# Performance work log

Hardware: AMD Instinct MI355X
Metric: run time of the kernel (lower is better)

Reference implementation:

```python
import jax, jax.numpy as jnp
import numpy as np

N = 50000   # nodes
E = 600000  # edges
H = 128     # hidden_dim


def _linear_params(key, fan_in, fan_out):
    kw, kb = jax.random.split(key)
    s = 1.0 / np.sqrt(fan_in)
    w = jax.random.uniform(kw, (fan_in, fan_out), minval=-s, maxval=s, dtype=jnp.float32)
    b = jax.random.uniform(kb, (fan_out,), minval=-s, maxval=s, dtype=jnp.float32)
    return w, b


def setup_inputs():
    key = jax.random.key(0)
    ks = jax.random.split(key, 9)
    x = jax.random.uniform(ks[0], (N, 1), dtype=jnp.float32)
    pre_h = jax.random.normal(ks[1], (N, H), dtype=jnp.float32)
    edge_index = jax.random.randint(ks[2], (2, E), 0, N, dtype=jnp.int32)
    edge_attr = jax.random.uniform(ks[3], (E, 1), dtype=jnp.float32)
    enc_w, enc_b = _linear_params(ks[4], 1 + H, H)      # BFS_Encoder.linear
    M_w, M_b = _linear_params(ks[5], H + H + 1, H)      # MPNN_Processor.M
    U_w, U_b = _linear_params(ks[6], H + H, H)          # MPNN_Processor.U
    dec_w, dec_b = _linear_params(ks[7], H + H, 1)      # BFS_Decoder.linear
    ter_w, ter_b = _linear_params(ks[8], H + H, 1)      # BFS_Terminator.linear
    return {"x": x, "pre_h": pre_h, "edge_attr": edge_attr,
            "enc_w": enc_w, "enc_b": enc_b, "M_w": M_w, "M_b": M_b,
            "U_w": U_w, "U_b": U_b, "dec_w": dec_w, "dec_b": dec_b,
            "ter_w": ter_w, "ter_b": ter_b, "edge_index": edge_index}


def reference(x, pre_h, edge_attr, enc_w, enc_b, M_w, M_b, U_w, U_b,
              dec_w, dec_b, ter_w, ter_b, edge_index):
    # Encoder: z = relu(Linear([x, pre_h]))
    z = jax.nn.relu(jnp.concatenate([x, pre_h], axis=-1) @ enc_w + enc_b)  # [N,H]

    # Processor (PyG MessagePassing, flow source_to_target):
    # z_i = z[edge_index[1]] (target), z_j = z[edge_index[0]] (source)
    src, tgt = edge_index[0], edge_index[1]
    m = jax.nn.relu(
        jnp.concatenate([z[tgt], z[src], edge_attr], axis=-1) @ M_w + M_b)  # [E,H]
    # scatter-max aggregate into target nodes; empty segments -> 0
    agg = jax.ops.segment_max(m, tgt, num_segments=N)
    agg = jnp.where(jnp.isfinite(agg), agg, 0.0)
    h = jax.nn.relu(jnp.concatenate([z, agg], axis=-1) @ U_w + U_b)  # [N,H]

    # Decoder
    y = jax.nn.sigmoid(jnp.concatenate([z, h], axis=-1) @ dec_w + dec_b)  # [N,1]

    # Terminator: mean over nodes, broadcast-concat, scalar mean
    h_mean = jnp.broadcast_to(jnp.mean(h, axis=0), h.shape)
    ter = jnp.mean(jnp.concatenate([h, h_mean], axis=-1) @ ter_w + ter_b)
    return h, y, ter
```

## Files before the change

### kernel.cpp

```cpp
#include <hip/hip_runtime.h>
#include <hip/hip_bf16.h>
#include <math.h>

#define HD 128
#define APAD 136
#define CAP 768

typedef short bf16x8 __attribute__((ext_vector_type(8)));
typedef float f32x4 __attribute__((ext_vector_type(4)));

static __device__ __forceinline__ unsigned short f2bf(float f) {
  __hip_bfloat16 b = __float2bfloat16(f);
  return *(unsigned short*)&b;
}
static __device__ __forceinline__ float bflo(unsigned int u) {
  return __uint_as_float(u << 16);
}
static __device__ __forceinline__ float bfhi(unsigned int u) {
  return __uint_as_float(u & 0xffff0000u);
}

__global__ __launch_bounds__(256) void k_frag(
    const float* __restrict__ enc_w, const float* __restrict__ M_w,
    const float* __restrict__ U_w,
    unsigned short* __restrict__ encf, unsigned short* __restrict__ Pf,
    unsigned short* __restrict__ Qf, unsigned short* __restrict__ Uf) {
  const int b = blockIdx.x;
  const float* W; unsigned short* F; int KS; int lb;
  if (b < 8)       { W = enc_w + HD;     F = encf; KS = 4; lb = b; }
  else if (b < 16) { W = M_w;            F = Pf;   KS = 4; lb = b - 8; }
  else if (b < 24) { W = M_w + HD * HD;  F = Qf;   KS = 4; lb = b - 16; }
  else             { W = U_w;            F = Uf;   KS = 8; lb = b - 24; }
  const int gid = lb * 256 + threadIdx.x;
  const int lane = gid & 63;
  const int ks = (gid >> 6) % KS;
  const int tile = gid / (64 * KS);
  const int col = tile * 16 + (lane & 15);
  const int k0 = ks * 32 + (lane >> 4) * 8;
  unsigned short v[8];
#pragma unroll
  for (int j = 0; j < 8; ++j) v[j] = f2bf(W[(size_t)(k0 + j) * HD + col]);
  unsigned short* dst = F + ((size_t)(tile * KS + ks) * 64 + lane) * 8;
#pragma unroll
  for (int j = 0; j < 8; ++j) dst[j] = v[j];
}

__global__ __launch_bounds__(256) void k_hist(
    const int* __restrict__ ei, int* __restrict__ cnt, int E) {
  const int e = blockIdx.x * 256 + threadIdx.x;
  if (e < E) atomicAdd(&cnt[ei[E + e]], 1);
}

__global__ __launch_bounds__(256) void k_scan_block(
    const int* __restrict__ cnt, int* __restrict__ row_ptr,
    int* __restrict__ partials, int N) {
  __shared__ int s[256];
  const int t = threadIdx.x;
  const int base = blockIdx.x * 1024 + t * 4;
  int v[4], sum = 0;
#pragma unroll
  for (int i = 0; i < 4; ++i) {
    v[i] = (base + i < N) ? cnt[base + i] : 0;
    sum += v[i];
  }
  s[t] = sum;
  __syncthreads();
  for (int off = 1; off < 256; off <<= 1) {
    int xv = (t >= off) ? s[t - off] : 0;
    __syncthreads();
    if (t >= off) s[t] += xv;
    __syncthreads();
  }
  int run = s[t] - sum;
  if (t == 255) partials[blockIdx.x] = s[255];
#pragma unroll
  for (int i = 0; i < 4; ++i) {
    if (base + i < N) row_ptr[base + i] = run;
    run += v[i];
  }
}

__global__ void k_scan_partials(int* __restrict__ partials, int nb) {
  if (threadIdx.x == 0) {
    int run = 0;
    for (int i = 0; i < nb; ++i) { int v = partials[i]; partials[i] = run; run += v; }
  }
}

__global__ __launch_bounds__(256) void k_scan_add(
    int* __restrict__ row_ptr, const int* __restrict__ partials,
    int* __restrict__ cursor, int N) {
  const int base = blockIdx.x * 1024 + threadIdx.x * 4;
  const int p = partials[blockIdx.x];
#pragma unroll
  for (int i = 0; i < 4; ++i) {
    if (base + i < N) {
      int v = row_ptr[base + i] + p;
      row_ptr[base + i] = v;
      cursor[base + i] = v;
    }
  }
}

__global__ __launch_bounds__(256) void k_scatter(
    const int* __restrict__ ei, const float* __restrict__ edge_attr,
    int* __restrict__ cursor, int2* __restrict__ epack, int E) {
  const int e = blockIdx.x * 256 + threadIdx.x;
  if (e >= E) return;
  const int tgt = ei[E + e];
  const int pos = atomicAdd(&cursor[tgt], 1);
  epack[pos] = make_int2(ei[e], __float_as_int(edge_attr[e]));
}

__global__ __launch_bounds__(256, 4) void k_enc_pq(
    const float* __restrict__ x, const float* __restrict__ pre_h,
    const float* __restrict__ enc_w, const float* __restrict__ enc_b,
    const float* __restrict__ M_b,
    const unsigned short* __restrict__ encf, const unsigned short* __restrict__ Pf,
    const unsigned short* __restrict__ Qf,
    unsigned short* __restrict__ zg, unsigned short* __restrict__ Pg,
    unsigned short* __restrict__ Qg) {
  __shared__ unsigned short phs[16 * APAD];
  __shared__ unsigned short zsh[16 * APAD];
  __shared__ float xs[16];
  const int t = threadIdx.x;
  const int n0 = blockIdx.x * 16;

  {
    const int r = t >> 4, c0 = (t & 15) * 8;
    const float4 a = *(const float4*)&pre_h[(size_t)(n0 + r) * HD + c0];
    const float4 b = *(const float4*)&pre_h[(size_t)(n0 + r) * HD + c0 + 4];
    unsigned short* d = &phs[r * APAD + c0];
    d[0] = f2bf(a.x); d[1] = f2bf(a.y); d[2] = f2bf(a.z); d[3] = f2bf(a.w);
    d[4] = f2bf(b.x); d[5] = f2bf(b.y); d[6] = f2bf(b.z); d[7] = f2bf(b.w);
  }
  if (t < 16) xs[t] = x[n0 + t];
  __syncthreads();

  const int w = t >> 6, l = t & 63;
  const int m = l & 15, q = l >> 4;

  bf16x8 af[4];
#pragma unroll
  for (int ks = 0; ks < 4; ++ks)
    af[ks] = *(const bf16x8*)&phs[m * APAD + ks * 32 + q * 8];
  f32x4 acc[2] = {{0, 0, 0, 0}, {0, 0, 0, 0}};
#pragma unroll
  for (int tt = 0; tt < 2; ++tt) {
    const int tn = 2 * w + tt;
#pragma unroll
    for (int ks = 0; ks < 4; ++ks) {
      const bf16x8 bf = *(const bf16x8*)&encf[((size_t)(tn * 4 + ks) * 64 + l) * 8];
      acc[tt] = __builtin_amdgcn_mfma_f32_16x16x32_bf16(af[ks], bf, acc[tt], 0, 0, 0);
    }
  }
#pragma unroll
  for (int tt = 0; tt < 2; ++tt) {
    const int col = (2 * w + tt) * 16 + m;
    const float bb = enc_b[col];
    const float w0 = enc_w[col];
#pragma unroll
    for (int r = 0; r < 4; ++r) {
      const int row = q * 4 + r;
      const float zv = fmaxf(acc[tt][r] + bb + xs[row] * w0, 0.0f);
      zsh[row * APAD + col] = f2bf(zv);
    }
  }
  __syncthreads();

  bf16x8 az[4];
#pragma unroll
  for (int ks = 0; ks < 4; ++ks)
    az[ks] = *(const bf16x8*)&zsh[m * APAD + ks * 32 + q * 8];
  {
    const int r = t >> 4, c0 = (t & 15) * 8;
    *(uint4*)&zg[(size_t)(n0 + r) * HD + c0] = *(const uint4*)&zsh[r * APAD + c0];
  }
  __syncthreads();

  f32x4 pacc[2] = {{0, 0, 0, 0}, {0, 0, 0, 0}};
  f32x4 qacc[2] = {{0, 0, 0, 0}, {0, 0, 0, 0}};
#pragma unroll
  for (int tt = 0; tt < 2; ++tt) {
    const int tn = 2 * w + tt;
#pragma unroll
    for (int ks = 0; ks < 4; ++ks) {
      const bf16x8 bp = *(const bf16x8*)&Pf[((size_t)(tn * 4 + ks) * 64 + l) * 8];
      const bf16x8 bq = *(const bf16x8*)&Qf[((size_t)(tn * 4 + ks) * 64 + l) * 8];
      pacc[tt] = __builtin_amdgcn_mfma_f32_16x16x32_bf16(az[ks], bp, pacc[tt], 0, 0, 0);
      qacc[tt] = __builtin_amdgcn_mfma_f32_16x16x32_bf16(az[ks], bq, qacc[tt], 0, 0, 0);
    }
  }
#pragma unroll
  for (int tt = 0; tt < 2; ++tt) {
    const int col = (2 * w + tt) * 16 + m;
    const float mb = M_b[col];
#pragma unroll
    for (int r = 0; r < 4; ++r) {
      const int row = q * 4 + r;
      phs[row * APAD + col] = f2bf(pacc[tt][r] + mb);
      zsh[row * APAD + col] = f2bf(qacc[tt][r]);
    }
  }
  __syncthreads();
  {
    const int r = t >> 4, c0 = (t & 15) * 8;
    *(uint4*)&Pg[(size_t)(n0 + r) * HD + c0] = *(const uint4*)&phs[r * APAD + c0];
    *(uint4*)&Qg[(size_t)(n0 + r) * HD + c0] = *(const uint4*)&zsh[r * APAD + c0];
  }
}

__global__ __launch_bounds__(256, 4) void k_gather_update(
    const unsigned short* __restrict__ zg, const unsigned short* __restrict__ Pg,
    const unsigned short* __restrict__ Qg, const float* __restrict__ w_attr,
    const int* __restrict__ row_ptr, const int* __restrict__ row_end,
    const int2* __restrict__ epack, const unsigned short* __restrict__ Uf,
    const float* __restrict__ U_b, const float* __restrict__ dec_w,
    const float* __restrict__ dec_b,
    float* __restrict__ h_out, float* __restrict__ y_out,
    float* __restrict__ hsum, int N) {
  __shared__ unsigned short zsh[32 * APAD];
  __shared__ unsigned short ash[32 * APAD];
  __shared__ int2 eL[CAP];
  __shared__ int rsL[32], reL[32];
  __shared__ float hcol[HD];
  __shared__ float dacc[32];
  __shared__ float pr[32][8];
  const int t = threadIdx.x;
  const int n0 = blockIdx.x * 32;

  {
    const int r = t >> 3, c0 = (t & 7) * 16;
    const int n = min(n0 + r, N - 1);
    *(uint4*)&zsh[r * APAD + c0]     = *(const uint4*)&zg[(size_t)n * HD + c0];
    *(uint4*)&zsh[r * APAD + c0 + 8] = *(const uint4*)&zg[(size_t)n * HD + c0 + 8];
  }
  if (t < 32) {
    const int n = min(n0 + t, N - 1);
    rsL[t] = row_ptr[n];
    reL[t] = row_end[n];
    dacc[t] = 0.0f;
  }
  if (t < HD) hcol[t] = 0.0f;
  __syncthreads();
  const int estart = rsL[0];
  const int ecnt = reL[31] - estart;
  for (int i = t; i < min(ecnt, CAP); i += 256) eL[i] = epack[estart + i];
  __syncthreads();

  const int w = t >> 6, l = t & 63;
  const int g = l >> 4, j = l & 15;

  float wv[8];
  {
    const float4 wa = *(const float4*)&w_attr[j * 8];
    const float4 wb = *(const float4*)&w_attr[j * 8 + 4];
    wv[0] = wa.x; wv[1] = wa.y; wv[2] = wa.z; wv[3] = wa.w;
    wv[4] = wb.x; wv[5] = wb.y; wv[6] = wb.z; wv[7] = wb.w;
  }
  const bool ovf = (ecnt > CAP);
#pragma unroll
  for (int i = 0; i < 2; ++i) {
    const int r = w * 8 + g * 2 + i;
    const int n = n0 + r;
    const int rs = rsL[r], re = reL[r];
    float acc[8];
#pragma unroll
    for (int c = 0; c < 8; ++c) acc[c] = -INFINITY;
    for (int e = rs; e < re; e += 4) {
      int ea[4];
      ea[0] = e;
      ea[1] = min(e + 1, re - 1);
      ea[2] = min(e + 2, re - 1);
      ea[3] = min(e + 3, re - 1);
      int2 pk[4];
#pragma unroll
      for (int u = 0; u < 4; ++u) {
        const int i0 = ea[u] - estart;
        pk[u] = (!ovf || i0 < CAP) ? eL[i0] : epack[ea[u]];
      }
      uint4 qv[4];
#pragma unroll
      for (int u = 0; u < 4; ++u)
        qv[u] = *(const uint4*)&Qg[(size_t)pk[u].x * HD + j * 8];
#pragma unroll
      for (int u = 0; u < 4; ++u) {
        const float a = __int_as_float(pk[u].y);
        const unsigned int qq[4] = {qv[u].x, qv[u].y, qv[u].z, qv[u].w};
#pragma unroll
        for (int c = 0; c < 4; ++c) {
          acc[2 * c]     = fmaxf(acc[2 * c],     fmaf(a, wv[2 * c],     bflo(qq[c])));
          acc[2 * c + 1] = fmaxf(acc[2 * c + 1], fmaf(a, wv[2 * c + 1], bfhi(qq[c])));
        }
      }
    }
    const bool valid = (n < N) && (re > rs);
    float res[8];
    if (valid) {
      const uint4 pv = *(const uint4*)&Pg[(size_t)n * HD + j * 8];
      const unsigned int pp[4] = {pv.x, pv.y, pv.z, pv.w};
#pragma unroll
      for (int c = 0; c < 4; ++c) {
        res[2 * c]     = fmaxf(bflo(pp[c]) + acc[2 * c],     0.0f);
        res[2 * c + 1] = fmaxf(bfhi(pp[c]) + acc[2 * c + 1], 0.0f);
      }
    } else {
#pragma unroll
      for (int c = 0; c < 8; ++c) res[c] = 0.0f;
    }
    uint4 st;
    st.x = (unsigned)f2bf(res[0]) | ((unsigned)f2bf(res[1]) << 16);
    st.y = (unsigned)f2bf(res[2]) | ((unsigned)f2bf(res[3]) << 16);
    st.z = (unsigned)f2bf(res[4]) | ((unsigned)f2bf(res[5]) << 16);
    st.w = (unsigned)f2bf(res[6]) | ((unsigned)f2bf(res[7]) << 16);
    *(uint4*)&ash[r * APAD + j * 8] = st;
  }
  __syncthreads();

  const int mt = w & 1, nh = w >> 1;
  const int m = mt * 16 + (l & 15), q = l >> 4;
  bf16x8 afz[4], afa[4];
#pragma unroll
  for (int ks = 0; ks < 4; ++ks) {
    afz[ks] = *(const bf16x8*)&zsh[m * APAD + ks * 32 + q * 8];
    afa[ks] = *(const bf16x8*)&ash[m * APAD + ks * 32 + q * 8];
  }
  f32x4 acc4[4] = {{0, 0, 0, 0}, {0, 0, 0, 0}, {0, 0, 0, 0}, {0, 0, 0, 0}};
#pragma unroll
  for (int tt = 0; tt < 4; ++tt) {
    const int tn = nh * 4 + tt;
#pragma unroll
    for (int ks = 0; ks < 8; ++ks) {
      const bf16x8 bf = *(const bf16x8*)&Uf[((size_t)(tn * 8 + ks) * 64 + l) * 8];
      const bf16x8 a = (ks < 4) ? afz[ks] : afa[ks - 4];
      acc4[tt] = __builtin_amdgcn_mfma_f32_16x16x32_bf16(a, bf, acc4[tt], 0, 0, 0);
    }
  }
  float dp[4] = {0.0f, 0.0f, 0.0f, 0.0f};
#pragma unroll
  for (int tt = 0; tt < 4; ++tt) {
    const int col = (nh * 4 + tt) * 16 + (l & 15);
    const float ub = U_b[col];
    const float dw = dec_w[HD + col];
    float s4 = 0.0f;
#pragma unroll
    for (int r = 0; r < 4; ++r) {
      const int rowl = mt * 16 + q * 4 + r;
      const int n = n0 + rowl;
      float hv = fmaxf(acc4[tt][r] + ub, 0.0f);
      if (n < N) h_out[(size_t)n * HD + col] = hv; else hv = 0.0f;
      s4 += hv;
      dp[r] += hv * dw;
    }
    atomicAdd(&hcol[col], s4);
  }
#pragma unroll
  for (int off = 1; off < 16; off <<= 1) {
#pragma unroll
    for (int r = 0; r < 4; ++r) dp[r] += __shfl_xor(dp[r], off);
  }
  if ((l & 15) == 0) {
#pragma unroll
    for (int r = 0; r < 4; ++r) atomicAdd(&dacc[mt * 16 + q * 4 + r], dp[r]);
  }

  {
    const int r2 = t >> 3, s = t & 7;
    float part = 0.0f;
#pragma unroll
    for (int c = 0; c < 8; ++c) {
      const int kk = s * 16 + 2 * c;
      const unsigned int zu = *(const unsigned int*)&zsh[r2 * APAD + kk];
      part += bflo(zu) * dec_w[kk] + bfhi(zu) * dec_w[kk + 1];
    }
    pr[r2][s] = part;
  }
  __syncthreads();

  if (t < HD) atomicAdd(&hsum[t], hcol[t]);
  if (t < 32 && n0 + t < N) {
    float d = dec_b[0] + dacc[t];
#pragma unroll
    for (int s = 0; s < 8; ++s) d += pr[t][s];
    y_out[n0 + t] = 1.0f / (1.0f + expf(-d));
  }
}

__global__ __launch_bounds__(128) void k_ter(
    const float* __restrict__ hsum, const float* __restrict__ ter_w,
    const float* __restrict__ ter_b, float* __restrict__ out, float invN) {
  __shared__ float r2[2];
  const int t = threadIdx.x;
  float v = (hsum[t] * invN) * (ter_w[t] + ter_w[HD + t]);
#pragma unroll
  for (int o = 32; o > 0; o >>= 1) v += __shfl_down(v, o);
  if ((t & 63) == 0) r2[t >> 6] = v;
  __syncthreads();
  if (t == 0) out[0] = r2[0] + r2[1] + ter_b[0];
}

extern "C" void kernel_launch(void* const* d_in, const int* in_sizes, int n_in,
                              void* d_out, int out_size, void* d_ws, size_t ws_size,
                              hipStream_t stream) {
  const float* x        = (const float*)d_in[0];
  const float* pre_h    = (const float*)d_in[1];
  const float* edge_attr= (const float*)d_in[2];
  const float* enc_w    = (const float*)d_in[3];
  const float* enc_b    = (const float*)d_in[4];
  const float* M_w      = (const float*)d_in[5];
  const float* M_b      = (const float*)d_in[6];
  const float* U_w      = (const float*)d_in[7];
  const float* U_b      = (const float*)d_in[8];
  const float* dec_w    = (const float*)d_in[9];
  const float* dec_b    = (const float*)d_in[10];
  const float* ter_w    = (const float*)d_in[11];
  const float* ter_b    = (const float*)d_in[12];
  const int*   edge_idx = (const int*)d_in[13];

  const int N = in_sizes[0];
  const int E = in_sizes[2];
  const size_t NH = (size_t)N * HD;

  float* out = (float*)d_out;
  float* h_out = out;
  float* y_out = out + NH;
  float* ter_out = out + NH + N;

  unsigned short* zg = (unsigned short*)d_ws;
  unsigned short* Pg = zg + NH;
  unsigned short* Qg = Pg + NH;
  int*   cursor   = (int*)(Qg + NH);
  int*   row_ptr  = cursor + N;
  int*   partials = row_ptr + N;
  float* hsum     = (float*)(partials + 64);
  int2*  epack    = (int2*)(hsum + HD);
  unsigned short* encf = (unsigned short*)(epack + E);
  unsigned short* Pf   = encf + 8 * 4 * 64 * 8;
  unsigned short* Qf   = Pf + 8 * 4 * 64 * 8;
  unsigned short* Uf   = Qf + 8 * 4 * 64 * 8;

  hipMemsetAsync(cursor, 0, (2 * (size_t)N + 64 + HD) * sizeof(int), stream);

  const int scan_blocks = (N + 1023) / 1024;
  const int eb = (E + 255) / 256;

  k_frag<<<40, 256, 0, stream>>>(enc_w, M_w, U_w, encf, Pf, Qf, Uf);

  k_hist<<<eb, 256, 0, stream>>>(edge_idx, cursor, E);
  k_scan_block<<<scan_blocks, 256, 0, stream>>>(cursor, row_ptr, partials, N);
  k_scan_partials<<<1, 64, 0, stream>>>(partials, scan_blocks);
  k_scan_add<<<scan_blocks, 256, 0, stream>>>(row_ptr, partials, cursor, N);
  k_scatter<<<eb, 256, 0, stream>>>(edge_idx, edge_attr, cursor, epack, E);

  k_enc_pq<<<N / 16, 256, 0, stream>>>(x, pre_h, enc_w, enc_b, M_b,
                                       encf, Pf, Qf, zg, Pg, Qg);
  k_gather_update<<<(N + 31) / 32, 256, 0, stream>>>(
      zg, Pg, Qg, M_w + 256 * HD, row_ptr, cursor, epack, Uf,
      U_b, dec_w, dec_b, h_out, y_out, hsum, N);
  k_ter<<<1, 128, 0, stream>>>(hsum, ter_w, ter_b, ter_out, 1.0f / (float)N);
}
```

Baseline: 263.1 us.

## Split gather from update kernel and merge weight-fragment prep with histogram

Result: slower. 274.0 us (+4.2%).

```diff
diff --git a/kernel.cpp b/kernel.cpp
--- a/kernel.cpp
+++ b/kernel.cpp
@@ -4,7 +4,6 @@
 
 #define HD 128
 #define APAD 136
-#define CAP 768
 
 typedef short bf16x8 __attribute__((ext_vector_type(8)));
 typedef float f32x4 __attribute__((ext_vector_type(4)));
@@ -20,12 +19,18 @@
   return __uint_as_float(u & 0xffff0000u);
 }
 
-__global__ __launch_bounds__(256) void k_frag(
+__global__ __launch_bounds__(256) void k_frag_hist(
     const float* __restrict__ enc_w, const float* __restrict__ M_w,
     const float* __restrict__ U_w,
     unsigned short* __restrict__ encf, unsigned short* __restrict__ Pf,
-    unsigned short* __restrict__ Qf, unsigned short* __restrict__ Uf) {
+    unsigned short* __restrict__ Qf, unsigned short* __restrict__ Uf,
+    const int* __restrict__ ei, int* __restrict__ cnt, int E) {
   const int b = blockIdx.x;
+  if (b >= 40) {
+    const int e = (b - 40) * 256 + threadIdx.x;
+    if (e < E) atomicAdd(&cnt[ei[E + e]], 1);
+    return;
+  }
   const float* W; unsigned short* F; int KS; int lb;
   if (b < 8)       { W = enc_w + HD;     F = encf; KS = 4; lb = b; }
   else if (b < 16) { W = M_w;            F = Pf;   KS = 4; lb = b - 8; }
@@ -43,12 +48,6 @@
   unsigned short* dst = F + ((size_t)(tile * KS + ks) * 64 + lane) * 8;
 #pragma unroll
   for (int j = 0; j < 8; ++j) dst[j] = v[j];
-}
-
-__global__ __launch_bounds__(256) void k_hist(
-    const int* __restrict__ ei, int* __restrict__ cnt, int E) {
-  const int e = blockIdx.x * 256 + threadIdx.x;
-  if (e < E) atomicAdd(&cnt[ei[E + e]], 1);
 }
 
 __global__ __launch_bounds__(256) void k_scan_block(
@@ -210,19 +209,86 @@
   }
 }
 
-__global__ __launch_bounds__(256, 4) void k_gather_update(
-    const unsigned short* __restrict__ zg, const unsigned short* __restrict__ Pg,
-    const unsigned short* __restrict__ Qg, const float* __restrict__ w_attr,
+__global__ __launch_bounds__(256, 6) void k_gather(
+    const unsigned short* __restrict__ Pg, const unsigned short* __restrict__ Qg,
+    const float* __restrict__ w_attr,
     const int* __restrict__ row_ptr, const int* __restrict__ row_end,
-    const int2* __restrict__ epack, const unsigned short* __restrict__ Uf,
+    const int2* __restrict__ epack,
+    unsigned short* __restrict__ ag, int N) {
+  const int t = threadIdx.x;
+  const int w = t >> 6, l = t & 63;
+  const int g = l >> 4, j = l & 15;
+  const int n0 = blockIdx.x * 32;
+
+  float wv[8];
+  {
+    const float4 wa = *(const float4*)&w_attr[j * 8];
+    const float4 wb = *(const float4*)&w_attr[j * 8 + 4];
+    wv[0] = wa.x; wv[1] = wa.y; wv[2] = wa.z; wv[3] = wa.w;
+    wv[4] = wb.x; wv[5] = wb.y; wv[6] = wb.z; wv[7] = wb.w;
+  }
+
+#pragma unroll
+  for (int i = 0; i < 2; ++i) {
+    const int r = w * 8 + g * 2 + i;
+    const int n = n0 + r;
+    const int nc = min(n, N - 1);
+    const int rs = row_ptr[nc], re = row_end[nc];
+    float acc[8];
+#pragma unroll
+    for (int c = 0; c < 8; ++c) acc[c] = -INFINITY;
+    for (int e = rs; e < re; e += 4) {
+      int2 pk[4];
+#pragma unroll
+      for (int u = 0; u < 4; ++u) pk[u] = epack[min(e + u, re - 1)];
+      uint4 qv[4];
+#pragma unroll
+      for (int u = 0; u < 4; ++u)
+        qv[u] = *(const uint4*)&Qg[(size_t)pk[u].x * HD + j * 8];
+#pragma unroll
+      for (int u = 0; u < 4; ++u) {
+        const float a = __int_as_float(pk[u].y);
+        const unsigned int qq[4] = {qv[u].x, qv[u].y, qv[u].z, qv[u].w};
+#pragma unroll
+        for (int c = 0; c < 4; ++c) {
+          acc[2 * c]     = fmaxf(acc[2 * c],     fmaf(a, wv[2 * c],     bflo(qq[c])));
+          acc[2 * c + 1] = fmaxf(acc[2 * c + 1], fmaf(a, wv[2 * c + 1], bfhi(qq[c])));
+        }
+      }
+    }
+    if (n < N) {
+      float res[8];
+      if (re > rs) {
+        const uint4 pv = *(const uint4*)&Pg[(size_t)n * HD + j * 8];
+        const unsigned int pp[4] = {pv.x, pv.y, pv.z, pv.w};
+#pragma unroll
+        for (int c = 0; c < 4; ++c) {
+          res[2 * c]     = fmaxf(bflo(pp[c]) + acc[2 * c],     0.0f);
+          res[2 * c + 1] = fmaxf(bfhi(pp[c]) + acc[2 * c + 1], 0.0f);
+        }
+      } else {
+#pragma unroll
+        for (int c = 0; c < 8; ++c) res[c] = 0.0f;
+      }
+      uint4 st;
+      st.x = (unsigned)f2bf(res[0]) | ((unsigned)f2bf(res[1]) << 16);
+      st.y = (unsigned)f2bf(res[2]) | ((unsigned)f2bf(res[3]) << 16);
+      st.z = (unsigned)f2bf(res[4]) | ((unsigned)f2bf(res[5]) << 16);
+      st.w = (unsigned)f2bf(res[6]) | ((unsigned)f2bf(res[7]) << 16);
+      *(uint4*)&ag[(size_t)n * HD + j * 8] = st;
+    }
+  }
+}
+
+__global__ __launch_bounds__(256, 4) void k_update(
+    const unsigned short* __restrict__ zg, const unsigned short* __restrict__ ag,
+    const unsigned short* __restrict__ Uf,
     const float* __restrict__ U_b, const float* __restrict__ dec_w,
     const float* __restrict__ dec_b,
     float* __restrict__ h_out, float* __restrict__ y_out,
     float* __restrict__ hsum, int N) {
   __shared__ unsigned short zsh[32 * APAD];
   __shared__ unsigned short ash[32 * APAD];
-  __shared__ int2 eL[CAP];
-  __shared__ int rsL[32], reL[32];
   __shared__ float hcol[HD];
   __shared__ float dacc[32];
   __shared__ float pr[32][8];
@@ -234,88 +300,14 @@
     const int n = min(n0 + r, N - 1);
     *(uint4*)&zsh[r * APAD + c0]     = *(const uint4*)&zg[(size_t)n * HD + c0];
     *(uint4*)&zsh[r * APAD + c0 + 8] = *(const uint4*)&zg[(size_t)n * HD + c0 + 8];
-  }
-  if (t < 32) {
-    const int n = min(n0 + t, N - 1);
-    rsL[t] = row_ptr[n];
-    reL[t] = row_end[n];
-    dacc[t] = 0.0f;
-  }
+    *(uint4*)&ash[r * APAD + c0]     = *(const uint4*)&ag[(size_t)n * HD + c0];
+    *(uint4*)&ash[r * APAD + c0 + 8] = *(const uint4*)&ag[(size_t)n * HD + c0 + 8];
+  }
+  if (t < 32) dacc[t] = 0.0f;
   if (t < HD) hcol[t] = 0.0f;
   __syncthreads();
-  const int estart = rsL[0];
-  const int ecnt = reL[31] - estart;
-  for (int i = t; i < min(ecnt, CAP); i += 256) eL[i] = epack[estart + i];
-  __syncthreads();
 
   const int w = t >> 6, l = t & 63;
-  const int g = l >> 4, j = l & 15;
-
-  float wv[8];
-  {
-    const float4 wa = *(const float4*)&w_attr[j * 8];
-    const float4 wb = *(const float4*)&w_attr[j * 8 + 4];
-    wv[0] = wa.x; wv[1] = wa.y; wv[2] = wa.z; wv[3] = wa.w;
-    wv[4] = wb.x; wv[5] = wb.y; wv[6] = wb.z; wv[7] = wb.w;
-  }
-  const bool ovf = (ecnt > CAP);
-#pragma unroll
-  for (int i = 0; i < 2; ++i) {
-    const int r = w * 8 + g * 2 + i;
-    const int n = n0 + r;
-    const int rs = rsL[r], re = reL[r];
-    float acc[8];
-#pragma unroll
-    for (int c = 0; c < 8; ++c) acc[c] = -INFINITY;
-    for (int e = rs; e < re; e += 4) {
-      int ea[4];
-      ea[0] = e;
-      ea[1] = min(e + 1, re - 1);
-      ea[2] = min(e + 2, re - 1);
-      ea[3] = min(e + 3, re - 1);
-      int2 pk[4];
-#pragma unroll
-      for (int u = 0; u < 4; ++u) {
-        const int i0 = ea[u] - estart;
-        pk[u] = (!ovf || i0 < CAP) ? eL[i0] : epack[ea[u]];
-      }
-      uint4 qv[4];
-#pragma unroll
-      for (int u = 0; u < 4; ++u)
-        qv[u] = *(const uint4*)&Qg[(size_t)pk[u].x * HD + j * 8];
-#pragma unroll
-      for (int u = 0; u < 4; ++u) {
-        const float a = __int_as_float(pk[u].y);
-        const unsigned int qq[4] = {qv[u].x, qv[u].y, qv[u].z, qv[u].w};
-#pragma unroll
-        for (int c = 0; c < 4; ++c) {
-          acc[2 * c]     = fmaxf(acc[2 * c],     fmaf(a, wv[2 * c],     bflo(qq[c])));
-          acc[2 * c + 1] = fmaxf(acc[2 * c + 1], fmaf(a, wv[2 * c + 1], bfhi(qq[c])));
-        }
-      }
-    }
-    const bool valid = (n < N) && (re > rs);
-    float res[8];
-    if (valid) {
-      const uint4 pv = *(const uint4*)&Pg[(size_t)n * HD + j * 8];
-      const unsigned int pp[4] = {pv.x, pv.y, pv.z, pv.w};
-#pragma unroll
-      for (int c = 0; c < 4; ++c) {
-        res[2 * c]     = fmaxf(bflo(pp[c]) + acc[2 * c],     0.0f);
-        res[2 * c + 1] = fmaxf(bfhi(pp[c]) + acc[2 * c + 1], 0.0f);
-      }
-    } else {
-#pragma unroll
-      for (int c = 0; c < 8; ++c) res[c] = 0.0f;
-    }
-    uint4 st;
-    st.x = (unsigned)f2bf(res[0]) | ((unsigned)f2bf(res[1]) << 16);
-    st.y = (unsigned)f2bf(res[2]) | ((unsigned)f2bf(res[3]) << 16);
-    st.z = (unsigned)f2bf(res[4]) | ((unsigned)f2bf(res[5]) << 16);
-    st.w = (unsigned)f2bf(res[6]) | ((unsigned)f2bf(res[7]) << 16);
-    *(uint4*)&ash[r * APAD + j * 8] = st;
-  }
-  __syncthreads();
 
   const int mt = w & 1, nh = w >> 1;
   const int m = mt * 16 + (l & 15), q = l >> 4;
@@ -429,7 +421,8 @@
   unsigned short* zg = (unsigned short*)d_ws;
   unsigned short* Pg = zg + NH;
   unsigned short* Qg = Pg + NH;
-  int*   cursor   = (int*)(Qg + NH);
+  unsigned short* ag = Qg + NH;
+  int*   cursor   = (int*)(ag + NH);
   int*   row_ptr  = cursor + N;
   int*   partials = row_ptr + N;
   float* hsum     = (float*)(partials + 64);
@@ -444,9 +437,8 @@
   const int scan_blocks = (N + 1023) / 1024;
   const int eb = (E + 255) / 256;
 
-  k_frag<<<40, 256, 0, stream>>>(enc_w, M_w, U_w, encf, Pf, Qf, Uf);
-
-  k_hist<<<eb, 256, 0, stream>>>(edge_idx, cursor, E);
+  k_frag_hist<<<40 + eb, 256, 0, stream>>>(enc_w, M_w, U_w, encf, Pf, Qf, Uf,
+                                           edge_idx, cursor, E);
   k_scan_block<<<scan_blocks, 256, 0, stream>>>(cursor, row_ptr, partials, N);
   k_scan_partials<<<1, 64, 0, stream>>>(partials, scan_blocks);
   k_scan_add<<<scan_blocks, 256, 0, stream>>>(row_ptr, partials, cursor, N);
@@ -454,8 +446,9 @@
 
   k_enc_pq<<<N / 16, 256, 0, stream>>>(x, pre_h, enc_w, enc_b, M_b,
                                        encf, Pf, Qf, zg, Pg, Qg);
-  k_gather_update<<<(N + 31) / 32, 256, 0, stream>>>(
-      zg, Pg, Qg, M_w + 256 * HD, row_ptr, cursor, epack, Uf,
-      U_b, dec_w, dec_b, h_out, y_out, hsum, N);
+  k_gather<<<(N + 31) / 32, 256, 0, stream>>>(
+      Pg, Qg, M_w + 256 * HD, row_ptr, cursor, epack, ag, N);
+  k_update<<<(N + 31) / 32, 256, 0, stream>>>(
+      zg, ag, Uf, U_b, dec_w, dec_b, h_out, y_out, hsum, N);
   k_ter<<<1, 128, 0, stream>>>(hsum, ter_w, ter_b, ter_out, 1.0f / (float)N);
 }
```
